# Optimization experiments

Measured on AMD Instinct MI355X. Metric: run time of the kernel, lower is better.

Reference implementation:

```python
import jax, jax.numpy as jnp
import numpy as np

THRESHOLD = 0.3
NEG_BIG = -2.0 ** 32  # matches tf -2**32 causal mask constant


def setup_inputs() -> dict:
    key = jax.random.key(0)
    kq, kt, kv = jax.random.split(key, 3)
    B, S, D = 16, 2048, 128
    Q = jax.random.normal(kq, (B, S, D), dtype=jnp.float32)
    T = jax.random.normal(kt, (B, S, D), dtype=jnp.float32)
    V = jax.random.normal(kv, (B, S, D), dtype=jnp.float32)
    return {"Q": Q, "T": T, "V": V}


def reference(Q, T, V):
    # scores: [B, S, S]
    A = jnp.einsum('bqd,bkd->bqk', Q, T)
    # Faithful to tf.where(A>thr, A, -2**32 * cast(A>thr)):
    # the false branch evaluates to 0 (mask is 0 there), NOT -2**32.
    A = jnp.where(A > THRESHOLD, A, jnp.zeros((), A.dtype))
    S = Q.shape[1]
    causal = jnp.triu(jnp.ones((S, S), dtype=bool), k=1)  # strictly upper = masked
    A = A + jnp.where(causal, jnp.asarray(NEG_BIG, A.dtype), jnp.zeros((), A.dtype))
    d_k = jnp.asarray(Q.shape[-1], A.dtype)
    A = A / jnp.sqrt(d_k)
    y = jax.nn.softmax(A, axis=-1)
    return jnp.einsum('bqk,bkd->bqd', y, V)
```

## Files before the change

### kernel.cpp

```cpp
#include <hip/hip_runtime.h>
#include <hip/hip_bf16.h>


#define S_LEN 2048
#define D_DIM 128
#define BQ 64
#define BK 64
#define THRESH 0.3f
#define SCALE 0.08838834764831845f

typedef __bf16 bf16x8 __attribute__((ext_vector_type(8)));
typedef float f32x4 __attribute__((ext_vector_type(4)));

#define GLD16(g, l)                                                         \
    __builtin_amdgcn_global_load_lds(                                       \
        (const __attribute__((address_space(1))) unsigned int*)(g),         \
        (__attribute__((address_space(3))) unsigned int*)(l), 16, 0, 0)

__global__ void prep_kernel(const float* __restrict__ V, const float* __restrict__ T,
                            __bf16* __restrict__ Vt, __bf16* __restrict__ Tb) {
    __shared__ float tile[64][65];
    int bid = blockIdx.x;
    int tid = threadIdx.x;
    int b  = bid >> 6;
    int t2 = bid & 63;

    {
        int flat = tid * 16;
        int r = flat >> 7, cc = flat & 127;
        const float* p = T + ((size_t)b * S_LEN + t2 * 32 + r) * D_DIM + cc;
        __bf16* q = Tb + ((size_t)b * S_LEN + t2 * 32 + r) * D_DIM + cc;
        bf16x8 w0, w1;
        f32x4 a0 = *(const f32x4*)p,       a1 = *(const f32x4*)(p + 4);
        f32x4 a2 = *(const f32x4*)(p + 8), a3 = *(const f32x4*)(p + 12);
        #pragma unroll
        for (int j = 0; j < 4; ++j) {
            w0[j] = (__bf16)a0[j]; w0[4 + j] = (__bf16)a1[j];
            w1[j] = (__bf16)a2[j]; w1[4 + j] = (__bf16)a3[j];
        }
        *(bf16x8*)q = w0;
        *(bf16x8*)(q + 8) = w1;
    }

    int s0 = (t2 >> 1) * 64;
    int d0 = (t2 & 1) * 64;
    #pragma unroll
    for (int it = 0; it < 2; ++it) {
        int row = it * 32 + (tid >> 3);
        int c   = (tid & 7) * 8;
        const float* p = V + ((size_t)b * S_LEN + s0 + row) * D_DIM + d0 + c;
        *(f32x4*)(&tile[row][c])     = *(const f32x4*)p;
        *(f32x4*)(&tile[row][c + 4]) = *(const f32x4*)(p + 4);
    }
    __syncthreads();
    #pragma unroll
    for (int it = 0; it < 2; ++it) {
        int dr = it * 32 + (tid >> 3);
        int c  = (tid & 7) * 8;
        bf16x8 w;
        #pragma unroll
        for (int j = 0; j < 8; ++j) w[j] = (__bf16)tile[c + j][dr];
        *(bf16x8*)(Vt + ((size_t)b * D_DIM + d0 + dr) * S_LEN + s0 + c) = w;
    }
}

__global__ __launch_bounds__(256, 2)
void fa_kernel(const float* __restrict__ Q, const __bf16* __restrict__ Tb,
               const __bf16* __restrict__ Vt, float* __restrict__ O,
               float* __restrict__ pO, float* __restrict__ pL) {
    __shared__ __align__(16) unsigned char smem[73728];

    const int bid = blockIdx.x;
    const int b   = bid & 15;
    const int pi  = (bid >> 4) & 15;
    const int c   = bid >> 8;
    const int qtH = 31 - pi;
    const int L   = pi + 1;

    const int tid  = threadIdx.x;
    const int lane = tid & 63;
    const int wv   = tid >> 6;
    const int col  = lane & 15;
    const int quad = lane >> 4;

    unsigned char* Pw = smem + 65536 + wv * 2048;

    const __bf16* TbB = Tb + (size_t)b * S_LEN * D_DIM;
    const __bf16* VtB = Vt + (size_t)b * D_DIM * S_LEN;

    int toff[4], voff[4];
    #pragma unroll
    for (int i = 0; i < 4; ++i) {
        int trw = wv * 16 + i * 4 + (lane >> 4);
        toff[i] = trw * 128 + (((lane & 15) ^ (trw & 7)) << 3);
        int drw = wv * 32 + i * 8 + (lane >> 3);
        voff[i] = drw * 2048 + (((lane & 7) ^ (drw & 7)) << 3);
    }

    auto issueTile = [&](int k0, int buf) {
        const __bf16* ts = TbB + (size_t)k0 * D_DIM;
        const __bf16* vs = VtB + k0;
        unsigned char* lt = smem + buf * 16384 + wv * 4096;
        unsigned char* lv = smem + 32768 + buf * 16384 + wv * 4096;
        #pragma unroll
        for (int i = 0; i < 4; ++i) GLD16(ts + toff[i], lt + i * 1024);
        #pragma unroll
        for (int i = 0; i < 4; ++i) GLD16(vs + voff[i], lv + i * 1024);
    };

    bf16x8 qf[4];
    auto loadQ = [&](int qt) {
        const float* qptr = Q + ((size_t)b * S_LEN + qt * BQ + wv * 16 + col) * D_DIM + quad * 8;
        #pragma unroll
        for (int kk = 0; kk < 4; ++kk) {
            f32x4 a = *(const f32x4*)(qptr + kk * 32);
            f32x4 d = *(const f32x4*)(qptr + kk * 32 + 4);
            #pragma unroll
            for (int j = 0; j < 4; ++j) { qf[kk][j] = (__bf16)a[j]; qf[kk][4 + j] = (__bf16)d[j]; }
        }
    };

    f32x4 oacc[8];
    float lsum[4];

    auto computeTile = [&](int buf, bool diag) {
        unsigned char* Tt = smem + buf * 16384;
        unsigned char* Vl = smem + 32768 + buf * 16384;
        f32x4 sacc[4];
        __builtin_amdgcn_s_setprio(1);
        #pragma unroll
        for (int t = 0; t < 4; ++t) {
            sacc[t] = {0.f, 0.f, 0.f, 0.f};
            #pragma unroll
            for (int kk = 0; kk < 4; ++kk) {
                int row = t * 16 + col;
                bf16x8 bf = *(const bf16x8*)(Tt + row * 256 + ((kk * 64 + quad * 16) ^ ((row & 7) << 4)));
                sacc[t] = __builtin_amdgcn_mfma_f32_16x16x32_bf16(qf[kk], bf, sacc[t], 0, 0, 0);
            }
        }
        __builtin_amdgcn_s_setprio(0);
        float p[4][4];
        #pragma unroll
        for (int t = 0; t < 4; ++t)
            #pragma unroll
            for (int r = 0; r < 4; ++r) {
                float s = sacc[t][r];
                float e = __expf(s * SCALE);
                float w = (s > THRESH) ? e : 1.0f;
                if (diag && (t * 16 + col > wv * 16 + quad * 4 + r)) w = 0.0f;
                p[t][r] = w;
            }
        #pragma unroll
        for (int r = 0; r < 4; ++r)
            lsum[r] += (p[0][r] + p[1][r]) + (p[2][r] + p[3][r]);

        #pragma unroll
        for (int t = 0; t < 4; ++t)
            #pragma unroll
            for (int r = 0; r < 4; ++r) {
                int row = quad * 4 + r;
                *(__bf16*)(Pw + row * 128 + (((t * 16 + col) * 2) ^ ((row & 7) << 4))) = (__bf16)p[t][r];
            }
        asm volatile("s_waitcnt lgkmcnt(0)" ::: "memory");

        __builtin_amdgcn_s_setprio(1);
        #pragma unroll
        for (int ks = 0; ks < 2; ++ks) {
            bf16x8 af = *(const bf16x8*)(Pw + col * 128 + ((ks * 64 + quad * 16) ^ ((col & 7) << 4)));
            #pragma unroll
            for (int dt = 0; dt < 8; ++dt) {
                int row = dt * 16 + col;
                bf16x8 bf = *(const bf16x8*)(Vl + row * 128 + ((ks * 64 + quad * 16) ^ ((row & 7) << 4)));
                oacc[dt] = __builtin_amdgcn_mfma_f32_16x16x32_bf16(af, bf, oacc[dt], 0, 0, 0);
            }
        }
        __builtin_amdgcn_s_setprio(0);
    };

    auto finishSeg = [&](int qt) {
        float lred[4];
        #pragma unroll
        for (int r = 0; r < 4; ++r) {
            float l = lsum[r];
            l += __shfl_xor(l, 1); l += __shfl_xor(l, 2);
            l += __shfl_xor(l, 4); l += __shfl_xor(l, 8);
            lred[r] = l;
        }
        if (qt < 16) {
            float* optr = O + ((size_t)b * S_LEN + qt * BQ + wv * 16) * D_DIM;
            #pragma unroll
            for (int dt = 0; dt < 8; ++dt)
                #pragma unroll
                for (int r = 0; r < 4; ++r)
                    optr[(quad * 4 + r) * D_DIM + dt * 16 + col] = oacc[dt][r] * (1.0f / lred[r]);
        } else {
            size_t slot = (size_t)((b * 16 + pi) * 2 + c);
            float* po = pO + slot * (64 * 128);
            float* pl = pL + slot * 64;
            #pragma unroll
            for (int dt = 0; dt < 8; ++dt)
                #pragma unroll
                for (int r = 0; r < 4; ++r)
                    po[(wv * 16 + quad * 4 + r) * 128 + dt * 16 + col] = oacc[dt][r];
            if (col == 0) {
                #pragma unroll
                for (int r = 0; r < 4; ++r) pl[wv * 16 + quad * 4 + r] = lred[r];
            }
        }
    };

    const int nseg = (c == 0) ? 2 : 1;
    for (int is = 0; is < nseg; ++is) {
        int qt, k0t, nt;
        if (c == 0) {
            if (is == 0) { qt = pi;  k0t = 0;      nt = L;      }
            else         { qt = qtH; k0t = 0;      nt = 17 - L; }
        } else           { qt = qtH; k0t = 17 - L; nt = 16;     }

        loadQ(qt);
        #pragma unroll
        for (int dt = 0; dt < 8; ++dt) oacc[dt] = {0.f, 0.f, 0.f, 0.f};
        #pragma unroll
        for (int r = 0; r < 4; ++r) lsum[r] = 0.f;

        issueTile(k0t * BK, 0);
        for (int s = 0; s < nt; ++s) {
            if (s + 1 < nt) {
                issueTile((k0t + s + 1) * BK, (s + 1) & 1);
                asm volatile("s_waitcnt vmcnt(8)" ::: "memory");
            } else {
                asm volatile("s_waitcnt vmcnt(0)" ::: "memory");
            }
            __builtin_amdgcn_s_barrier();
            computeTile(s & 1, k0t + s == qt);
            __builtin_amdgcn_s_barrier();
        }
        finishSeg(qt);
    }
}

__global__ void nrm_kernel(const float* __restrict__ pO, const float* __restrict__ pL,
                           float* __restrict__ O) {
    int gid  = blockIdx.x * 256 + threadIdx.x;
    int flat = gid * 16;
    int pr   = flat >> 13;
    int rl   = (flat >> 7) & 63;
    int cc   = flat & 127;
    int b = pr >> 4, pi = pr & 15;
    const float* p0 = pO + ((size_t)pr * 2)     * 8192 + rl * 128 + cc;
    const float* p1 = pO + ((size_t)pr * 2 + 1) * 8192 + rl * 128 + cc;
    float inv = 1.0f / (pL[(pr * 2) * 64 + rl] + pL[(pr * 2 + 1) * 64 + rl]);
    float* op = O + ((size_t)b * S_LEN + (31 - pi) * 64 + rl) * D_DIM + cc;
    #pragma unroll
    for (int j = 0; j < 4; ++j) {
        f32x4 a = *(const f32x4*)(p0 + j * 4);
        f32x4 d = *(const f32x4*)(p1 + j * 4);
        f32x4 o;
        #pragma unroll
        for (int r = 0; r < 4; ++r) o[r] = (a[r] + d[r]) * inv;
        *(f32x4*)(op + j * 4) = o;
    }
}

extern "C" void kernel_launch(void* const* d_in, const int* in_sizes, int n_in,
                              void* d_out, int out_size, void* d_ws, size_t ws_size,
                              hipStream_t stream) {
    const float* Q = (const float*)d_in[0];
    const float* T = (const float*)d_in[1];
    const float* V = (const float*)d_in[2];
    float* O = (float*)d_out;

    unsigned char* ws = (unsigned char*)d_ws;
    __bf16* Vt = (__bf16*)ws;
    __bf16* Tb = (__bf16*)(ws + 8388608);
    float*  pO = (float*)(ws + 16777216);
    float*  pL = (float*)(ws + 16777216 + 16777216);

    prep_kernel<<<1024, 256, 0, stream>>>(V, T, Vt, Tb);
    fa_kernel<<<512, 256, 0, stream>>>(Q, Tb, Vt, O, pO, pL);
    nrm_kernel<<<512, 256, 0, stream>>>(pO, pL, O);
}
```

Measured before the change: 132.4 us.

## Switch to 32x32 MFMA with 128-row query tiles and in-kernel split-K reduction

Moves the attention kernel from 16x16x32 to 32x32x16 bf16 MFMA with 128-query-row tiles per block. The P tile now stays in registers as the A operand instead of round-tripping through LDS. The work split changes to four chunks per query-pair, and partial outputs are stored in bf16. The separate normalization kernel is gone: the last block spin-waits on atomic counters (zeroed in prep) and sums the partials itself. This removes a launch and fp32 partial traffic, but adds inter-block spin-waiting that could deadlock if blocks are not co-resident, plus bf16 rounding of the partials.

```diff
diff --git a/kernel.cpp b/kernel.cpp
--- a/kernel.cpp
+++ b/kernel.cpp
@@ -4,13 +4,14 @@
 
 #define S_LEN 2048
 #define D_DIM 128
-#define BQ 64
-#define BK 64
 #define THRESH 0.3f
 #define SCALE 0.08838834764831845f
 
 typedef __bf16 bf16x8 __attribute__((ext_vector_type(8)));
 typedef float f32x4 __attribute__((ext_vector_type(4)));
+typedef float f32x16 __attribute__((ext_vector_type(16)));
+typedef unsigned long long u64;
+typedef unsigned long long u64x2 __attribute__((ext_vector_type(2)));
 
 #define GLD16(g, l)                                                         \
     __builtin_amdgcn_global_load_lds(                                       \
@@ -18,10 +19,12 @@
         (__attribute__((address_space(3))) unsigned int*)(l), 16, 0, 0)
 
 __global__ void prep_kernel(const float* __restrict__ V, const float* __restrict__ T,
-                            __bf16* __restrict__ Vt, __bf16* __restrict__ Tb) {
+                            __bf16* __restrict__ Vt, __bf16* __restrict__ Tb,
+                            int* __restrict__ done) {
     __shared__ float tile[64][65];
     int bid = blockIdx.x;
     int tid = threadIdx.x;
+    if (bid == 0) done[tid] = 0;
     int b  = bid >> 6;
     int t2 = bid & 63;
 
@@ -67,26 +70,25 @@
 __global__ __launch_bounds__(256, 2)
 void fa_kernel(const float* __restrict__ Q, const __bf16* __restrict__ Tb,
                const __bf16* __restrict__ Vt, float* __restrict__ O,
-               float* __restrict__ pO, float* __restrict__ pL) {
-    __shared__ __align__(16) unsigned char smem[73728];
+               __bf16* __restrict__ pO, float* __restrict__ pL,
+               int* __restrict__ done) {
+    __shared__ __align__(16) unsigned char smem[65536];
 
     const int bid = blockIdx.x;
     const int b   = bid & 15;
-    const int pi  = (bid >> 4) & 15;
-    const int c   = bid >> 8;
-    const int qtH = 31 - pi;
-    const int L   = pi + 1;
+    const int pi  = (bid >> 4) & 7;
+    const int c   = bid >> 7;
+    const int L2  = 2 * pi + 2;
+    const int pr  = b * 8 + pi;
 
     const int tid  = threadIdx.x;
     const int lane = tid & 63;
     const int wv   = tid >> 6;
-    const int col  = lane & 15;
-    const int quad = lane >> 4;
-
-    unsigned char* Pw = smem + 65536 + wv * 2048;
-
-    const __bf16* TbB = Tb + (size_t)b * S_LEN * D_DIM;
-    const __bf16* VtB = Vt + (size_t)b * D_DIM * S_LEN;
+    const int l31  = lane & 31;
+    const int hi   = lane >> 5;
+
+    const __bf16* TbB = Tb + (size_t)b * (S_LEN * D_DIM);
+    const __bf16* VtB = Vt + (size_t)b * (D_DIM * S_LEN);
 
     int toff[4], voff[4];
     #pragma unroll
@@ -108,157 +110,196 @@
         for (int i = 0; i < 4; ++i) GLD16(vs + voff[i], lv + i * 1024);
     };
 
-    bf16x8 qf[4];
-    auto loadQ = [&](int qt) {
-        const float* qptr = Q + ((size_t)b * S_LEN + qt * BQ + wv * 16 + col) * D_DIM + quad * 8;
-        #pragma unroll
-        for (int kk = 0; kk < 4; ++kk) {
-            f32x4 a = *(const f32x4*)(qptr + kk * 32);
-            f32x4 d = *(const f32x4*)(qptr + kk * 32 + 4);
+    bf16x8 qf[8];
+    auto loadQ = [&](int jq) {
+        const float* qptr = Q + ((size_t)b * S_LEN + jq * 128 + wv * 32 + l31) * D_DIM + hi * 8;
+        #pragma unroll
+        for (int kk = 0; kk < 8; ++kk) {
+            f32x4 a = *(const f32x4*)(qptr + kk * 16);
+            f32x4 d = *(const f32x4*)(qptr + kk * 16 + 4);
             #pragma unroll
             for (int j = 0; j < 4; ++j) { qf[kk][j] = (__bf16)a[j]; qf[kk][4 + j] = (__bf16)d[j]; }
         }
     };
 
-    f32x4 oacc[8];
-    float lsum[4];
-
-    auto computeTile = [&](int buf, bool diag) {
+    f32x16 oacc[4];
+    float  lsum;
+
+    auto computeTile = [&](int buf, int jq, int kt) {
         unsigned char* Tt = smem + buf * 16384;
         unsigned char* Vl = smem + 32768 + buf * 16384;
-        f32x4 sacc[4];
+        f32x16 sacc0 = {}, sacc1 = {};
         __builtin_amdgcn_s_setprio(1);
         #pragma unroll
-        for (int t = 0; t < 4; ++t) {
-            sacc[t] = {0.f, 0.f, 0.f, 0.f};
-            #pragma unroll
-            for (int kk = 0; kk < 4; ++kk) {
-                int row = t * 16 + col;
-                bf16x8 bf = *(const bf16x8*)(Tt + row * 256 + ((kk * 64 + quad * 16) ^ ((row & 7) << 4)));
-                sacc[t] = __builtin_amdgcn_mfma_f32_16x16x32_bf16(qf[kk], bf, sacc[t], 0, 0, 0);
+        for (int kk = 0; kk < 8; ++kk) {
+            int r0 = l31;
+            bf16x8 tf0 = *(const bf16x8*)(Tt + r0 * 256 + ((kk * 32 + hi * 16) ^ ((r0 & 7) << 4)));
+            sacc0 = __builtin_amdgcn_mfma_f32_32x32x16_bf16(tf0, qf[kk], sacc0, 0, 0, 0);
+            int r1 = 32 + l31;
+            bf16x8 tf1 = *(const bf16x8*)(Tt + r1 * 256 + ((kk * 32 + hi * 16) ^ ((r1 & 7) << 4)));
+            sacc1 = __builtin_amdgcn_mfma_f32_32x32x16_bf16(tf1, qf[kk], sacc1, 0, 0, 0);
+        }
+        __builtin_amdgcn_s_setprio(0);
+
+        const int qin = wv * 32 + l31;
+        const int dK  = 128 * jq - 64 * kt;
+        float p[2][16];
+        #pragma unroll
+        for (int g = 0; g < 16; ++g) {
+            float s0 = sacc0[g], s1 = sacc1[g];
+            float e0 = __expf(s0 * SCALE), e1 = __expf(s1 * SCALE);
+            p[0][g] = (s0 > THRESH) ? e0 : 1.0f;
+            p[1][g] = (s1 > THRESH) ? e1 : 1.0f;
+        }
+        if (dK < 64) {
+            #pragma unroll
+            for (int t = 0; t < 2; ++t)
+                #pragma unroll
+                for (int g = 0; g < 16; ++g) {
+                    int key = t * 32 + (g & 3) + 8 * (g >> 2) + 4 * hi;
+                    if (key - qin > dK) p[t][g] = 0.0f;
+                }
+        }
+        float ls = 0.f;
+        #pragma unroll
+        for (int g = 0; g < 16; ++g) ls += (p[0][g] + p[1][g]);
+        lsum += ls;
+
+        bf16x8 pka[4];
+        #pragma unroll
+        for (int ks = 0; ks < 4; ++ks)
+            #pragma unroll
+            for (int j = 0; j < 8; ++j)
+                pka[ks][j] = (__bf16)p[ks >> 1][8 * (ks & 1) + j];
+
+        __builtin_amdgcn_s_setprio(1);
+        #pragma unroll
+        for (int ks = 0; ks < 4; ++ks) {
+            #pragma unroll
+            for (int dt = 0; dt < 4; ++dt) {
+                int d = dt * 32 + l31;
+                u64x2 vv;
+                vv[0] = *(const u64*)(Vl + d * 128 + ((((2 * ks)     ^ (d & 7)) << 4) + 8 * hi));
+                vv[1] = *(const u64*)(Vl + d * 128 + ((((2 * ks + 1) ^ (d & 7)) << 4) + 8 * hi));
+                bf16x8 vf = __builtin_bit_cast(bf16x8, vv);
+                oacc[dt] = __builtin_amdgcn_mfma_f32_32x32x16_bf16(pka[ks], vf, oacc[dt], 0, 0, 0);
             }
         }
         __builtin_amdgcn_s_setprio(0);
-        float p[4][4];
-        #pragma unroll
-        for (int t = 0; t < 4; ++t)
-            #pragma unroll
-            for (int r = 0; r < 4; ++r) {
-                float s = sacc[t][r];
-                float e = __expf(s * SCALE);
-                float w = (s > THRESH) ? e : 1.0f;
-                if (diag && (t * 16 + col > wv * 16 + quad * 4 + r)) w = 0.0f;
-                p[t][r] = w;
-            }
-        #pragma unroll
-        for (int r = 0; r < 4; ++r)
-            lsum[r] += (p[0][r] + p[1][r]) + (p[2][r] + p[3][r]);
-
-        #pragma unroll
-        for (int t = 0; t < 4; ++t)
-            #pragma unroll
-            for (int r = 0; r < 4; ++r) {
-                int row = quad * 4 + r;
-                *(__bf16*)(Pw + row * 128 + (((t * 16 + col) * 2) ^ ((row & 7) << 4))) = (__bf16)p[t][r];
-            }
-        asm volatile("s_waitcnt lgkmcnt(0)" ::: "memory");
-
-        __builtin_amdgcn_s_setprio(1);
-        #pragma unroll
-        for (int ks = 0; ks < 2; ++ks) {
-            bf16x8 af = *(const bf16x8*)(Pw + col * 128 + ((ks * 64 + quad * 16) ^ ((col & 7) << 4)));
-            #pragma unroll
-            for (int dt = 0; dt < 8; ++dt) {
-                int row = dt * 16 + col;
-                bf16x8 bf = *(const bf16x8*)(Vl + row * 128 + ((ks * 64 + quad * 16) ^ ((row & 7) << 4)));
-                oacc[dt] = __builtin_amdgcn_mfma_f32_16x16x32_bf16(af, bf, oacc[dt], 0, 0, 0);
-            }
-        }
-        __builtin_amdgcn_s_setprio(0);
-    };
-
-    auto finishSeg = [&](int qt) {
-        float lred[4];
-        #pragma unroll
-        for (int r = 0; r < 4; ++r) {
-            float l = lsum[r];
-            l += __shfl_xor(l, 1); l += __shfl_xor(l, 2);
-            l += __shfl_xor(l, 4); l += __shfl_xor(l, 8);
-            lred[r] = l;
-        }
-        if (qt < 16) {
-            float* optr = O + ((size_t)b * S_LEN + qt * BQ + wv * 16) * D_DIM;
-            #pragma unroll
-            for (int dt = 0; dt < 8; ++dt)
-                #pragma unroll
-                for (int r = 0; r < 4; ++r)
-                    optr[(quad * 4 + r) * D_DIM + dt * 16 + col] = oacc[dt][r] * (1.0f / lred[r]);
-        } else {
-            size_t slot = (size_t)((b * 16 + pi) * 2 + c);
-            float* po = pO + slot * (64 * 128);
-            float* pl = pL + slot * 64;
-            #pragma unroll
-            for (int dt = 0; dt < 8; ++dt)
-                #pragma unroll
-                for (int r = 0; r < 4; ++r)
-                    po[(wv * 16 + quad * 4 + r) * 128 + dt * 16 + col] = oacc[dt][r];
-            if (col == 0) {
-                #pragma unroll
-                for (int r = 0; r < 4; ++r) pl[wv * 16 + quad * 4 + r] = lred[r];
-            }
-        }
-    };
-
-    const int nseg = (c == 0) ? 2 : 1;
-    for (int is = 0; is < nseg; ++is) {
-        int qt, k0t, nt;
-        if (c == 0) {
-            if (is == 0) { qt = pi;  k0t = 0;      nt = L;      }
-            else         { qt = qtH; k0t = 0;      nt = 17 - L; }
-        } else           { qt = qtH; k0t = 17 - L; nt = 16;     }
-
-        loadQ(qt);
-        #pragma unroll
-        for (int dt = 0; dt < 8; ++dt) oacc[dt] = {0.f, 0.f, 0.f, 0.f};
-        #pragma unroll
-        for (int r = 0; r < 4; ++r) lsum[r] = 0.f;
-
-        issueTile(k0t * BK, 0);
+    };
+
+    auto runSeg = [&](int jq, int k0t, int nt) {
+        loadQ(jq);
+        f32x16 z = {};
+        #pragma unroll
+        for (int dt = 0; dt < 4; ++dt) oacc[dt] = z;
+        lsum = 0.f;
+        issueTile(k0t * 64, 0);
         for (int s = 0; s < nt; ++s) {
             if (s + 1 < nt) {
-                issueTile((k0t + s + 1) * BK, (s + 1) & 1);
+                issueTile((k0t + s + 1) * 64, (s + 1) & 1);
                 asm volatile("s_waitcnt vmcnt(8)" ::: "memory");
             } else {
                 asm volatile("s_waitcnt vmcnt(0)" ::: "memory");
             }
             __builtin_amdgcn_s_barrier();
-            computeTile(s & 1, k0t + s == qt);
+            computeTile(s & 1, jq, k0t + s);
             __builtin_amdgcn_s_barrier();
         }
-        finishSeg(qt);
-    }
-}
-
-__global__ void nrm_kernel(const float* __restrict__ pO, const float* __restrict__ pL,
-                           float* __restrict__ O) {
-    int gid  = blockIdx.x * 256 + threadIdx.x;
-    int flat = gid * 16;
-    int pr   = flat >> 13;
-    int rl   = (flat >> 7) & 63;
-    int cc   = flat & 127;
-    int b = pr >> 4, pi = pr & 15;
-    const float* p0 = pO + ((size_t)pr * 2)     * 8192 + rl * 128 + cc;
-    const float* p1 = pO + ((size_t)pr * 2 + 1) * 8192 + rl * 128 + cc;
-    float inv = 1.0f / (pL[(pr * 2) * 64 + rl] + pL[(pr * 2 + 1) * 64 + rl]);
-    float* op = O + ((size_t)b * S_LEN + (31 - pi) * 64 + rl) * D_DIM + cc;
-    #pragma unroll
-    for (int j = 0; j < 4; ++j) {
-        f32x4 a = *(const f32x4*)(p0 + j * 4);
-        f32x4 d = *(const f32x4*)(p1 + j * 4);
-        f32x4 o;
-        #pragma unroll
-        for (int r = 0; r < 4; ++r) o[r] = (a[r] + d[r]) * inv;
-        *(f32x4*)(op + j * 4) = o;
+    };
+
+    auto reduceL = [&]() -> float { return lsum + __shfl_xor(lsum, 32); };
+
+    auto storeOfinal = [&](int jq, float l_all) {
+        float linv = 1.0f / l_all;
+        float* optr = O + ((size_t)b * S_LEN + jq * 128 + wv * 32) * D_DIM;
+        #pragma unroll
+        for (int g = 0; g < 16; ++g) {
+            int ql = (g & 3) + 8 * (g >> 2) + 4 * hi;
+            float iv = __shfl(linv, ql);
+            #pragma unroll
+            for (int dt = 0; dt < 4; ++dt)
+                optr[ql * D_DIM + dt * 32 + l31] = oacc[dt][g] * iv;
+        }
+    };
+
+    auto storePartial = [&](int slot, float l_all, int* dcnt) {
+        __bf16* po = pO + (size_t)(pr * 3 + slot) * (128 * 128);
+        float*  pl = pL + (size_t)(pr * 3 + slot) * 128;
+        #pragma unroll
+        for (int g = 0; g < 16; ++g) {
+            int row = wv * 32 + (g & 3) + 8 * (g >> 2) + 4 * hi;
+            #pragma unroll
+            for (int dt = 0; dt < 4; ++dt)
+                po[row * 128 + dt * 32 + l31] = (__bf16)oacc[dt][g];
+        }
+        if (lane < 32) pl[wv * 32 + lane] = l_all;
+        __threadfence();
+        __syncthreads();
+        if (tid == 0)
+            __hip_atomic_fetch_add(dcnt, 1, __ATOMIC_RELEASE, __HIP_MEMORY_SCOPE_AGENT);
+    };
+
+    auto addPartial = [&](int slot, float* l_all) {
+        const __bf16* po = pO + (size_t)(pr * 3 + slot) * (128 * 128);
+        const float*  pl = pL + (size_t)(pr * 3 + slot) * 128;
+        #pragma unroll
+        for (int g = 0; g < 16; ++g) {
+            int row = wv * 32 + (g & 3) + 8 * (g >> 2) + 4 * hi;
+            #pragma unroll
+            for (int dt = 0; dt < 4; ++dt)
+                oacc[dt][g] += (float)po[row * 128 + dt * 32 + l31];
+        }
+        *l_all += pl[wv * 32 + l31];
+    };
+
+    auto spinFor = [&](int* dcnt, int need) {
+        if (tid == 0) {
+            while (__hip_atomic_load(dcnt, __ATOMIC_ACQUIRE, __HIP_MEMORY_SCOPE_AGENT) < need)
+                __builtin_amdgcn_s_sleep(8);
+        }
+        __syncthreads();
+        __threadfence();
+    };
+
+    if (c == 0) {
+        if (pi <= 3) {
+            runSeg(pi, 0, L2);
+            storeOfinal(pi, reduceL());
+            runSeg(15 - pi, 0, 9 - L2);
+            float lh = reduceL();
+            storePartial(0, lh, &done[128 + pr]);
+        } else {
+            runSeg(pi, 0, 9);
+            float la = reduceL();
+            storePartial(0, la, &done[pr]);
+        }
+    } else if (c == 1) {
+        if (pi <= 3) {
+            runSeg(15 - pi, 9 - L2, 8);
+            float lh = reduceL();
+            storePartial(1, lh, &done[128 + pr]);
+        } else {
+            runSeg(15 - pi, 0, 17 - L2);
+            float lh = reduceL();
+            storePartial(1, lh, &done[128 + pr]);
+            runSeg(pi, 9, L2 - 9);
+            float la = reduceL();
+            spinFor(&done[pr], 1);
+            addPartial(0, &la);
+            storeOfinal(pi, la);
+        }
+    } else if (c == 2) {
+        runSeg(15 - pi, 17 - L2, 9);
+        float lh = reduceL();
+        storePartial(2, lh, &done[128 + pr]);
+    } else {
+        runSeg(15 - pi, 26 - L2, 8);
+        float lh = reduceL();
+        int s0 = (pi <= 3) ? 0 : 1;
+        spinFor(&done[128 + pr], 3 - s0);
+        for (int s = s0; s < 3; ++s) addPartial(s, &lh);
+        storeOfinal(15 - pi, lh);
     }
 }
 
@@ -273,10 +314,10 @@
     unsigned char* ws = (unsigned char*)d_ws;
     __bf16* Vt = (__bf16*)ws;
     __bf16* Tb = (__bf16*)(ws + 8388608);
-    float*  pO = (float*)(ws + 16777216);
-    float*  pL = (float*)(ws + 16777216 + 16777216);
-
-    prep_kernel<<<1024, 256, 0, stream>>>(V, T, Vt, Tb);
-    fa_kernel<<<512, 256, 0, stream>>>(Q, Tb, Vt, O, pO, pL);
-    nrm_kernel<<<512, 256, 0, stream>>>(pO, pL, O);
+    __bf16* pO = (__bf16*)(ws + 16777216);
+    float*  pL = (float*)(ws + 16777216 + 12582912);
+    int*  done = (int*)(ws + 16777216 + 12582912 + 196608);
+
+    prep_kernel<<<1024, 256, 0, stream>>>(V, T, Vt, Tb, done);
+    fa_kernel<<<512, 256, 0, stream>>>(Q, Tb, Vt, O, pO, pL, done);
 }
```

Result: slower. 205.5 us (+55.2%).

## Use 128-row query tiles with 8 waves and in-kernel split-K reduction via atomics

Applied to the files above, without the earlier changes.

Each block now uses 512 threads and covers a 128-row query tile, with work split into four chunks per pair of low/high query tiles. Partial outputs are written in bf16, and a completion counter plus spin-wait lets the last block merge them in-kernel, which removes the separate normalization kernel. The larger Q tile halves how often T/V tiles are reloaded, and the bf16 partials cut workspace traffic. The costs are 80KB of LDS, spin-wait dependencies that rely on the producer blocks being co-resident, and reduced precision in the partial sums.

```diff
diff --git a/kernel.cpp b/kernel.cpp
--- a/kernel.cpp
+++ b/kernel.cpp
@@ -4,8 +4,6 @@
 
 #define S_LEN 2048
 #define D_DIM 128
-#define BQ 64
-#define BK 64
 #define THRESH 0.3f
 #define SCALE 0.08838834764831845f
 
@@ -18,10 +16,12 @@
         (__attribute__((address_space(3))) unsigned int*)(l), 16, 0, 0)
 
 __global__ void prep_kernel(const float* __restrict__ V, const float* __restrict__ T,
-                            __bf16* __restrict__ Vt, __bf16* __restrict__ Tb) {
+                            __bf16* __restrict__ Vt, __bf16* __restrict__ Tb,
+                            int* __restrict__ done) {
     __shared__ float tile[64][65];
     int bid = blockIdx.x;
     int tid = threadIdx.x;
+    if (bid == 0) done[tid] = 0;
     int b  = bid >> 6;
     int t2 = bid & 63;
 
@@ -64,18 +64,20 @@
     }
 }
 
-__global__ __launch_bounds__(256, 2)
+__global__ __launch_bounds__(512, 4)
 void fa_kernel(const float* __restrict__ Q, const __bf16* __restrict__ Tb,
                const __bf16* __restrict__ Vt, float* __restrict__ O,
-               float* __restrict__ pO, float* __restrict__ pL) {
-    __shared__ __align__(16) unsigned char smem[73728];
+               __bf16* __restrict__ pO, float* __restrict__ pL,
+               int* __restrict__ done) {
+    __shared__ __align__(16) unsigned char smem[81920];
 
     const int bid = blockIdx.x;
     const int b   = bid & 15;
-    const int pi  = (bid >> 4) & 15;
-    const int c   = bid >> 8;
-    const int qtH = 31 - pi;
-    const int L   = pi + 1;
+    const int pi  = (bid >> 4) & 7;
+    const int c   = bid >> 7;
+    const int L2  = 2 * pi + 2;
+    const int pr  = b * 8 + pi;
+    const int qtL = pi, qtH = 15 - pi;
 
     const int tid  = threadIdx.x;
     const int lane = tid & 63;
@@ -84,33 +86,32 @@
     const int quad = lane >> 4;
 
     unsigned char* Pw = smem + 65536 + wv * 2048;
-
-    const __bf16* TbB = Tb + (size_t)b * S_LEN * D_DIM;
-    const __bf16* VtB = Vt + (size_t)b * D_DIM * S_LEN;
-
-    int toff[4], voff[4];
+    const __bf16* TbB = Tb + (size_t)b * (S_LEN * D_DIM);
+    const __bf16* VtB = Vt + (size_t)b * (D_DIM * S_LEN);
+
+    int toff[2], voff[2];
     #pragma unroll
-    for (int i = 0; i < 4; ++i) {
-        int trw = wv * 16 + i * 4 + (lane >> 4);
+    for (int i = 0; i < 2; ++i) {
+        int trw = wv * 8 + i * 4 + (lane >> 4);
         toff[i] = trw * 128 + (((lane & 15) ^ (trw & 7)) << 3);
-        int drw = wv * 32 + i * 8 + (lane >> 3);
+        int drw = wv * 16 + i * 8 + (lane >> 3);
         voff[i] = drw * 2048 + (((lane & 7) ^ (drw & 7)) << 3);
     }
 
     auto issueTile = [&](int k0, int buf) {
         const __bf16* ts = TbB + (size_t)k0 * D_DIM;
         const __bf16* vs = VtB + k0;
-        unsigned char* lt = smem + buf * 16384 + wv * 4096;
-        unsigned char* lv = smem + 32768 + buf * 16384 + wv * 4096;
-        #pragma unroll
-        for (int i = 0; i < 4; ++i) GLD16(ts + toff[i], lt + i * 1024);
-        #pragma unroll
-        for (int i = 0; i < 4; ++i) GLD16(vs + voff[i], lv + i * 1024);
+        unsigned char* lt = smem + buf * 16384 + wv * 2048;
+        unsigned char* lv = smem + 32768 + buf * 16384 + wv * 2048;
+        GLD16(ts + toff[0], lt);
+        GLD16(ts + toff[1], lt + 1024);
+        GLD16(vs + voff[0], lv);
+        GLD16(vs + voff[1], lv + 1024);
     };
 
     bf16x8 qf[4];
-    auto loadQ = [&](int qt) {
-        const float* qptr = Q + ((size_t)b * S_LEN + qt * BQ + wv * 16 + col) * D_DIM + quad * 8;
+    auto loadQ = [&](int jq) {
+        const float* qptr = Q + ((size_t)b * S_LEN + jq * 128 + wv * 16 + col) * D_DIM + quad * 8;
         #pragma unroll
         for (int kk = 0; kk < 4; ++kk) {
             f32x4 a = *(const f32x4*)(qptr + kk * 32);
@@ -123,7 +124,7 @@
     f32x4 oacc[8];
     float lsum[4];
 
-    auto computeTile = [&](int buf, bool diag) {
+    auto computeTile = [&](int buf, int dK) {
         unsigned char* Tt = smem + buf * 16384;
         unsigned char* Vl = smem + 32768 + buf * 16384;
         f32x4 sacc[4];
@@ -146,10 +147,15 @@
             for (int r = 0; r < 4; ++r) {
                 float s = sacc[t][r];
                 float e = __expf(s * SCALE);
-                float w = (s > THRESH) ? e : 1.0f;
-                if (diag && (t * 16 + col > wv * 16 + quad * 4 + r)) w = 0.0f;
-                p[t][r] = w;
-            }
+                p[t][r] = (s > THRESH) ? e : 1.0f;
+            }
+        if (dK < 64) {
+            #pragma unroll
+            for (int t = 0; t < 4; ++t)
+                #pragma unroll
+                for (int r = 0; r < 4; ++r)
+                    if (t * 16 + col - (wv * 16 + quad * 4 + r) > dK) p[t][r] = 0.0f;
+        }
         #pragma unroll
         for (int r = 0; r < 4; ++r)
             lsum[r] += (p[0][r] + p[1][r]) + (p[2][r] + p[3][r]);
@@ -177,8 +183,28 @@
         __builtin_amdgcn_s_setprio(0);
     };
 
-    auto finishSeg = [&](int qt) {
-        float lred[4];
+    auto runSeg = [&](int jq, int k0t, int nt) {
+        loadQ(jq);
+        #pragma unroll
+        for (int dt = 0; dt < 8; ++dt) oacc[dt] = {0.f, 0.f, 0.f, 0.f};
+        #pragma unroll
+        for (int r = 0; r < 4; ++r) lsum[r] = 0.f;
+        issueTile(k0t * 64, 0);
+        for (int s = 0; s < nt; ++s) {
+            if (s + 1 < nt) {
+                issueTile((k0t + s + 1) * 64, (s + 1) & 1);
+                asm volatile("s_waitcnt vmcnt(4)" ::: "memory");
+            } else {
+                asm volatile("s_waitcnt vmcnt(0)" ::: "memory");
+            }
+            __builtin_amdgcn_s_barrier();
+            computeTile(s & 1, 128 * jq - 64 * (k0t + s));
+            __builtin_amdgcn_s_barrier();
+        }
+    };
+
+    float lred[4];
+    auto reduceL = [&]() {
         #pragma unroll
         for (int r = 0; r < 4; ++r) {
             float l = lsum[r];
@@ -186,79 +212,97 @@
             l += __shfl_xor(l, 4); l += __shfl_xor(l, 8);
             lred[r] = l;
         }
-        if (qt < 16) {
-            float* optr = O + ((size_t)b * S_LEN + qt * BQ + wv * 16) * D_DIM;
+    };
+
+    auto storeO = [&](int jq) {
+        float* optr = O + ((size_t)b * S_LEN + jq * 128 + wv * 16) * D_DIM;
+        #pragma unroll
+        for (int r = 0; r < 4; ++r) {
+            float inv = 1.0f / lred[r];
             #pragma unroll
             for (int dt = 0; dt < 8; ++dt)
-                #pragma unroll
-                for (int r = 0; r < 4; ++r)
-                    optr[(quad * 4 + r) * D_DIM + dt * 16 + col] = oacc[dt][r] * (1.0f / lred[r]);
+                optr[(quad * 4 + r) * D_DIM + dt * 16 + col] = oacc[dt][r] * inv;
+        }
+    };
+
+    auto storePartial = [&](int slot, int* dcnt) {
+        __bf16* po = pO + (size_t)(pr * 4 + slot) * (128 * 128);
+        float*  pl = pL + (size_t)(pr * 4 + slot) * 128;
+        #pragma unroll
+        for (int dt = 0; dt < 8; ++dt)
+            #pragma unroll
+            for (int r = 0; r < 4; ++r)
+                po[(wv * 16 + quad * 4 + r) * 128 + dt * 16 + col] = (__bf16)oacc[dt][r];
+        if (col == 0) {
+            #pragma unroll
+            for (int r = 0; r < 4; ++r) pl[wv * 16 + quad * 4 + r] = lred[r];
+        }
+        __threadfence();
+        __syncthreads();
+        if (tid == 0)
+            __hip_atomic_fetch_add(dcnt, 1, __ATOMIC_RELEASE, __HIP_MEMORY_SCOPE_AGENT);
+    };
+
+    auto addPartial = [&](int slot) {
+        const __bf16* po = pO + (size_t)(pr * 4 + slot) * (128 * 128);
+        const float*  pl = pL + (size_t)(pr * 4 + slot) * 128;
+        #pragma unroll
+        for (int dt = 0; dt < 8; ++dt)
+            #pragma unroll
+            for (int r = 0; r < 4; ++r)
+                oacc[dt][r] += (float)po[(wv * 16 + quad * 4 + r) * 128 + dt * 16 + col];
+        #pragma unroll
+        for (int r = 0; r < 4; ++r) lred[r] += pl[wv * 16 + quad * 4 + r];
+    };
+
+    auto spinFor = [&](int* dcnt, int need) {
+        if (tid == 0) {
+            while (__hip_atomic_load(dcnt, __ATOMIC_ACQUIRE, __HIP_MEMORY_SCOPE_AGENT) < need)
+                __builtin_amdgcn_s_sleep(8);
+        }
+        __syncthreads();
+        __threadfence();
+    };
+
+    if (c == 0) {
+        if (pi <= 3) {
+            runSeg(qtL, 0, L2);
+            reduceL();
+            storeO(qtL);
+            runSeg(qtH, 0, 9 - L2);
+            reduceL();
+            storePartial(0, &done[128 + pr]);
         } else {
-            size_t slot = (size_t)((b * 16 + pi) * 2 + c);
-            float* po = pO + slot * (64 * 128);
-            float* pl = pL + slot * 64;
-            #pragma unroll
-            for (int dt = 0; dt < 8; ++dt)
-                #pragma unroll
-                for (int r = 0; r < 4; ++r)
-                    po[(wv * 16 + quad * 4 + r) * 128 + dt * 16 + col] = oacc[dt][r];
-            if (col == 0) {
-                #pragma unroll
-                for (int r = 0; r < 4; ++r) pl[wv * 16 + quad * 4 + r] = lred[r];
-            }
-        }
-    };
-
-    const int nseg = (c == 0) ? 2 : 1;
-    for (int is = 0; is < nseg; ++is) {
-        int qt, k0t, nt;
-        if (c == 0) {
-            if (is == 0) { qt = pi;  k0t = 0;      nt = L;      }
-            else         { qt = qtH; k0t = 0;      nt = 17 - L; }
-        } else           { qt = qtH; k0t = 17 - L; nt = 16;     }
-
-        loadQ(qt);
-        #pragma unroll
-        for (int dt = 0; dt < 8; ++dt) oacc[dt] = {0.f, 0.f, 0.f, 0.f};
-        #pragma unroll
-        for (int r = 0; r < 4; ++r) lsum[r] = 0.f;
-
-        issueTile(k0t * BK, 0);
-        for (int s = 0; s < nt; ++s) {
-            if (s + 1 < nt) {
-                issueTile((k0t + s + 1) * BK, (s + 1) & 1);
-                asm volatile("s_waitcnt vmcnt(8)" ::: "memory");
-            } else {
-                asm volatile("s_waitcnt vmcnt(0)" ::: "memory");
-            }
-            __builtin_amdgcn_s_barrier();
-            computeTile(s & 1, k0t + s == qt);
-            __builtin_amdgcn_s_barrier();
-        }
-        finishSeg(qt);
-    }
-}
-
-__global__ void nrm_kernel(const float* __restrict__ pO, const float* __restrict__ pL,
-                           float* __restrict__ O) {
-    int gid  = blockIdx.x * 256 + threadIdx.x;
-    int flat = gid * 16;
-    int pr   = flat >> 13;
-    int rl   = (flat >> 7) & 63;
-    int cc   = flat & 127;
-    int b = pr >> 4, pi = pr & 15;
-    const float* p0 = pO + ((size_t)pr * 2)     * 8192 + rl * 128 + cc;
-    const float* p1 = pO + ((size_t)pr * 2 + 1) * 8192 + rl * 128 + cc;
-    float inv = 1.0f / (pL[(pr * 2) * 64 + rl] + pL[(pr * 2 + 1) * 64 + rl]);
-    float* op = O + ((size_t)b * S_LEN + (31 - pi) * 64 + rl) * D_DIM + cc;
-    #pragma unroll
-    for (int j = 0; j < 4; ++j) {
-        f32x4 a = *(const f32x4*)(p0 + j * 4);
-        f32x4 d = *(const f32x4*)(p1 + j * 4);
-        f32x4 o;
-        #pragma unroll
-        for (int r = 0; r < 4; ++r) o[r] = (a[r] + d[r]) * inv;
-        *(f32x4*)(op + j * 4) = o;
+            runSeg(qtL, 0, 9);
+            reduceL();
+            storePartial(3, &done[pr]);
+        }
+    } else if (c == 1) {
+        if (pi <= 3) {
+            runSeg(qtH, 9 - L2, 8);
+            reduceL();
+            storePartial(1, &done[128 + pr]);
+        } else {
+            runSeg(qtH, 0, 17 - L2);
+            reduceL();
+            storePartial(1, &done[128 + pr]);
+            runSeg(qtL, 9, L2 - 9);
+            reduceL();
+            spinFor(&done[pr], 1);
+            addPartial(3);
+            storeO(qtL);
+        }
+    } else if (c == 2) {
+        runSeg(qtH, 17 - L2, 9);
+        reduceL();
+        storePartial(2, &done[128 + pr]);
+    } else {
+        runSeg(qtH, 26 - L2, 8);
+        reduceL();
+        int s0 = (pi <= 3) ? 0 : 1;
+        spinFor(&done[128 + pr], 3 - s0);
+        for (int s = s0; s < 3; ++s) addPartial(s);
+        storeO(qtH);
     }
 }
 
@@ -273,10 +317,10 @@
     unsigned char* ws = (unsigned char*)d_ws;
     __bf16* Vt = (__bf16*)ws;
     __bf16* Tb = (__bf16*)(ws + 8388608);
-    float*  pO = (float*)(ws + 16777216);
+    __bf16* pO = (__bf16*)(ws + 16777216);
     float*  pL = (float*)(ws + 16777216 + 16777216);
-
-    prep_kernel<<<1024, 256, 0, stream>>>(V, T, Vt, Tb);
-    fa_kernel<<<512, 256, 0, stream>>>(Q, Tb, Vt, O, pO, pL);
-    nrm_kernel<<<512, 256, 0, stream>>>(pO, pL, O);
+    int*  done = (int*)(ws + 16777216 + 16777216 + 262144);
+
+    prep_kernel<<<1024, 256, 0, stream>>>(V, T, Vt, Tb, done);
+    fa_kernel<<<512, 512, 0, stream>>>(Q, Tb, Vt, O, pO, pL, done);
 }
```

Result: slower. 317.0 us (+139.4%).

## Repartition attention tile so each wave owns key columns and D-slice

Applied to the files above, without the earlier changes.

Work is re-split across the four waves. Each wave now computes transposed scores for its own 16 keys against all 64 queries, with Q held in registers for all four query sub-tiles. P is written to one shared LDS tile, and each wave then computes a 32-wide slice of the output D dimension for all queries. This cuts per-wave LDS reads of T and V fragments and reuses each loaded fragment across four MFMAs. In exchange it adds an extra block barrier per tile, a cross-wave row-sum reduction through LDS, and higher register pressure from 16 Q fragments.

```diff
diff --git a/kernel.cpp b/kernel.cpp
--- a/kernel.cpp
+++ b/kernel.cpp
@@ -4,12 +4,11 @@
 
 #define S_LEN 2048
 #define D_DIM 128
-#define BQ 64
-#define BK 64
 #define THRESH 0.3f
 #define SCALE 0.08838834764831845f
 
 typedef __bf16 bf16x8 __attribute__((ext_vector_type(8)));
+typedef __bf16 bf16x4 __attribute__((ext_vector_type(4)));
 typedef float f32x4 __attribute__((ext_vector_type(4)));
 
 #define GLD16(g, l)                                                         \
@@ -83,10 +82,11 @@
     const int col  = lane & 15;
     const int quad = lane >> 4;
 
-    unsigned char* Pw = smem + 65536 + wv * 2048;
-
-    const __bf16* TbB = Tb + (size_t)b * S_LEN * D_DIM;
-    const __bf16* VtB = Vt + (size_t)b * D_DIM * S_LEN;
+    unsigned char* Pb = smem + 65536;
+    float* Lxf = (float*)(smem + 65536);
+
+    const __bf16* TbB = Tb + (size_t)b * (S_LEN * D_DIM);
+    const __bf16* VtB = Vt + (size_t)b * (D_DIM * S_LEN);
 
     int toff[4], voff[4];
     #pragma unroll
@@ -108,37 +108,43 @@
         for (int i = 0; i < 4; ++i) GLD16(vs + voff[i], lv + i * 1024);
     };
 
-    bf16x8 qf[4];
-    auto loadQ = [&](int qt) {
-        const float* qptr = Q + ((size_t)b * S_LEN + qt * BQ + wv * 16 + col) * D_DIM + quad * 8;
-        #pragma unroll
-        for (int kk = 0; kk < 4; ++kk) {
-            f32x4 a = *(const f32x4*)(qptr + kk * 32);
-            f32x4 d = *(const f32x4*)(qptr + kk * 32 + 4);
-            #pragma unroll
-            for (int j = 0; j < 4; ++j) { qf[kk][j] = (__bf16)a[j]; qf[kk][4 + j] = (__bf16)d[j]; }
-        }
-    };
-
-    f32x4 oacc[8];
+    bf16x8 qf[4][4];
+    auto loadQ = [&](int jq) {
+        #pragma unroll
+        for (int t = 0; t < 4; ++t) {
+            const float* qptr = Q + ((size_t)b * S_LEN + jq * 64 + 16 * t + col) * D_DIM + quad * 8;
+            #pragma unroll
+            for (int kk = 0; kk < 4; ++kk) {
+                f32x4 a = *(const f32x4*)(qptr + kk * 32);
+                f32x4 d = *(const f32x4*)(qptr + kk * 32 + 4);
+                #pragma unroll
+                for (int j = 0; j < 4; ++j) { qf[t][kk][j] = (__bf16)a[j]; qf[t][kk][4 + j] = (__bf16)d[j]; }
+            }
+        }
+    };
+
+    f32x4 oacc[4][2];
     float lsum[4];
+    float lfull[4][4];
 
     auto computeTile = [&](int buf, bool diag) {
         unsigned char* Tt = smem + buf * 16384;
         unsigned char* Vl = smem + 32768 + buf * 16384;
+
         f32x4 sacc[4];
+        #pragma unroll
+        for (int t = 0; t < 4; ++t) sacc[t] = {0.f, 0.f, 0.f, 0.f};
         __builtin_amdgcn_s_setprio(1);
         #pragma unroll
-        for (int t = 0; t < 4; ++t) {
-            sacc[t] = {0.f, 0.f, 0.f, 0.f};
-            #pragma unroll
-            for (int kk = 0; kk < 4; ++kk) {
-                int row = t * 16 + col;
-                bf16x8 bf = *(const bf16x8*)(Tt + row * 256 + ((kk * 64 + quad * 16) ^ ((row & 7) << 4)));
-                sacc[t] = __builtin_amdgcn_mfma_f32_16x16x32_bf16(qf[kk], bf, sacc[t], 0, 0, 0);
-            }
+        for (int kk = 0; kk < 4; ++kk) {
+            int trow = wv * 16 + col;
+            bf16x8 tf = *(const bf16x8*)(Tt + trow * 256 + ((kk * 64 + quad * 16) ^ ((trow & 7) << 4)));
+            #pragma unroll
+            for (int t = 0; t < 4; ++t)
+                sacc[t] = __builtin_amdgcn_mfma_f32_16x16x32_bf16(tf, qf[t][kk], sacc[t], 0, 0, 0);
         }
         __builtin_amdgcn_s_setprio(0);
+
         float p[4][4];
         #pragma unroll
         for (int t = 0; t < 4; ++t)
@@ -146,96 +152,134 @@
             for (int r = 0; r < 4; ++r) {
                 float s = sacc[t][r];
                 float e = __expf(s * SCALE);
-                float w = (s > THRESH) ? e : 1.0f;
-                if (diag && (t * 16 + col > wv * 16 + quad * 4 + r)) w = 0.0f;
-                p[t][r] = w;
-            }
-        #pragma unroll
-        for (int r = 0; r < 4; ++r)
-            lsum[r] += (p[0][r] + p[1][r]) + (p[2][r] + p[3][r]);
-
-        #pragma unroll
-        for (int t = 0; t < 4; ++t)
-            #pragma unroll
-            for (int r = 0; r < 4; ++r) {
-                int row = quad * 4 + r;
-                *(__bf16*)(Pw + row * 128 + (((t * 16 + col) * 2) ^ ((row & 7) << 4))) = (__bf16)p[t][r];
-            }
+                p[t][r] = (s > THRESH) ? e : 1.0f;
+            }
+        if (diag) {
+            #pragma unroll
+            for (int t = 0; t < 4; ++t)
+                #pragma unroll
+                for (int r = 0; r < 4; ++r)
+                    if (wv * 16 + quad * 4 + r > 16 * t + col) p[t][r] = 0.0f;
+        }
+        #pragma unroll
+        for (int t = 0; t < 4; ++t)
+            lsum[t] += (p[t][0] + p[t][1]) + (p[t][2] + p[t][3]);
+
+        #pragma unroll
+        for (int t = 0; t < 4; ++t) {
+            int row = 16 * t + col;
+            bf16x4 w = {(__bf16)p[t][0], (__bf16)p[t][1], (__bf16)p[t][2], (__bf16)p[t][3]};
+            *(bf16x4*)(Pb + row * 128 + ((32 * wv + 8 * quad) ^ ((row & 7) << 4))) = w;
+        }
         asm volatile("s_waitcnt lgkmcnt(0)" ::: "memory");
+        __builtin_amdgcn_s_barrier();
 
         __builtin_amdgcn_s_setprio(1);
         #pragma unroll
-        for (int ks = 0; ks < 2; ++ks) {
-            bf16x8 af = *(const bf16x8*)(Pw + col * 128 + ((ks * 64 + quad * 16) ^ ((col & 7) << 4)));
-            #pragma unroll
-            for (int dt = 0; dt < 8; ++dt) {
-                int row = dt * 16 + col;
-                bf16x8 bf = *(const bf16x8*)(Vl + row * 128 + ((ks * 64 + quad * 16) ^ ((row & 7) << 4)));
-                oacc[dt] = __builtin_amdgcn_mfma_f32_16x16x32_bf16(af, bf, oacc[dt], 0, 0, 0);
+        for (int kb = 0; kb < 2; ++kb) {
+            bf16x8 pf[4];
+            #pragma unroll
+            for (int t = 0; t < 4; ++t) {
+                int prow = 16 * t + col;
+                pf[t] = *(const bf16x8*)(Pb + prow * 128 + ((kb * 64 + quad * 16) ^ ((prow & 7) << 4)));
+            }
+            #pragma unroll
+            for (int dn = 0; dn < 2; ++dn) {
+                int vrow = 32 * wv + 16 * dn + col;
+                bf16x8 vf = *(const bf16x8*)(Vl + vrow * 128 + ((kb * 64 + quad * 16) ^ ((vrow & 7) << 4)));
+                #pragma unroll
+                for (int t = 0; t < 4; ++t)
+                    oacc[t][dn] = __builtin_amdgcn_mfma_f32_16x16x32_bf16(pf[t], vf, oacc[t][dn], 0, 0, 0);
             }
         }
         __builtin_amdgcn_s_setprio(0);
     };
 
-    auto finishSeg = [&](int qt) {
-        float lred[4];
-        #pragma unroll
-        for (int r = 0; r < 4; ++r) {
-            float l = lsum[r];
-            l += __shfl_xor(l, 1); l += __shfl_xor(l, 2);
-            l += __shfl_xor(l, 4); l += __shfl_xor(l, 8);
-            lred[r] = l;
-        }
-        if (qt < 16) {
-            float* optr = O + ((size_t)b * S_LEN + qt * BQ + wv * 16) * D_DIM;
-            #pragma unroll
-            for (int dt = 0; dt < 8; ++dt)
-                #pragma unroll
-                for (int r = 0; r < 4; ++r)
-                    optr[(quad * 4 + r) * D_DIM + dt * 16 + col] = oacc[dt][r] * (1.0f / lred[r]);
-        } else {
-            size_t slot = (size_t)((b * 16 + pi) * 2 + c);
-            float* po = pO + slot * (64 * 128);
-            float* pl = pL + slot * 64;
-            #pragma unroll
-            for (int dt = 0; dt < 8; ++dt)
-                #pragma unroll
-                for (int r = 0; r < 4; ++r)
-                    po[(wv * 16 + quad * 4 + r) * 128 + dt * 16 + col] = oacc[dt][r];
-            if (col == 0) {
-                #pragma unroll
-                for (int r = 0; r < 4; ++r) pl[wv * 16 + quad * 4 + r] = lred[r];
-            }
-        }
-    };
-
-    const int nseg = (c == 0) ? 2 : 1;
-    for (int is = 0; is < nseg; ++is) {
-        int qt, k0t, nt;
-        if (c == 0) {
-            if (is == 0) { qt = pi;  k0t = 0;      nt = L;      }
-            else         { qt = qtH; k0t = 0;      nt = 17 - L; }
-        } else           { qt = qtH; k0t = 17 - L; nt = 16;     }
-
-        loadQ(qt);
-        #pragma unroll
-        for (int dt = 0; dt < 8; ++dt) oacc[dt] = {0.f, 0.f, 0.f, 0.f};
-        #pragma unroll
-        for (int r = 0; r < 4; ++r) lsum[r] = 0.f;
-
-        issueTile(k0t * BK, 0);
+    auto runSeg = [&](int jq, int k0t, int nt) {
+        loadQ(jq);
+        #pragma unroll
+        for (int t = 0; t < 4; ++t) {
+            oacc[t][0] = {0.f, 0.f, 0.f, 0.f};
+            oacc[t][1] = {0.f, 0.f, 0.f, 0.f};
+            lsum[t] = 0.f;
+        }
+        issueTile(k0t * 64, 0);
         for (int s = 0; s < nt; ++s) {
             if (s + 1 < nt) {
-                issueTile((k0t + s + 1) * BK, (s + 1) & 1);
+                issueTile((k0t + s + 1) * 64, (s + 1) & 1);
                 asm volatile("s_waitcnt vmcnt(8)" ::: "memory");
             } else {
                 asm volatile("s_waitcnt vmcnt(0)" ::: "memory");
             }
             __builtin_amdgcn_s_barrier();
-            computeTile(s & 1, k0t + s == qt);
+            computeTile(s & 1, k0t + s == jq);
             __builtin_amdgcn_s_barrier();
         }
-        finishSeg(qt);
+    };
+
+    auto finishSeg = [&]() {
+        #pragma unroll
+        for (int t = 0; t < 4; ++t) {
+            float lw = lsum[t];
+            lw += __shfl_xor(lw, 16);
+            lw += __shfl_xor(lw, 32);
+            if (quad == 0) Lxf[wv * 64 + 16 * t + col] = lw;
+        }
+        __syncthreads();
+        #pragma unroll
+        for (int t = 0; t < 4; ++t)
+            #pragma unroll
+            for (int r = 0; r < 4; ++r) {
+                int q = 16 * t + quad * 4 + r;
+                lfull[t][r] = (Lxf[q] + Lxf[64 + q]) + (Lxf[128 + q] + Lxf[192 + q]);
+            }
+        __syncthreads();
+    };
+
+    auto storeO = [&](int jq) {
+        float* optr = O + ((size_t)b * S_LEN + jq * 64) * D_DIM;
+        #pragma unroll
+        for (int t = 0; t < 4; ++t)
+            #pragma unroll
+            for (int r = 0; r < 4; ++r) {
+                float inv = 1.0f / lfull[t][r];
+                #pragma unroll
+                for (int dn = 0; dn < 2; ++dn)
+                    optr[(16 * t + quad * 4 + r) * D_DIM + 32 * wv + 16 * dn + col] = oacc[t][dn][r] * inv;
+            }
+    };
+
+    auto storePartial = [&]() {
+        size_t slot = (size_t)((b * 16 + pi) * 2 + c);
+        float* po = pO + slot * (64 * 128);
+        float* pl = pL + slot * 64;
+        #pragma unroll
+        for (int t = 0; t < 4; ++t)
+            #pragma unroll
+            for (int r = 0; r < 4; ++r)
+                #pragma unroll
+                for (int dn = 0; dn < 2; ++dn)
+                    po[(16 * t + quad * 4 + r) * 128 + 32 * wv + 16 * dn + col] = oacc[t][dn][r];
+        if (wv == 0 && col == 0) {
+            #pragma unroll
+            for (int t = 0; t < 4; ++t)
+                #pragma unroll
+                for (int r = 0; r < 4; ++r)
+                    pl[16 * t + quad * 4 + r] = lfull[t][r];
+        }
+    };
+
+    if (c == 0) {
+        runSeg(pi, 0, L);
+        finishSeg();
+        storeO(pi);
+        runSeg(qtH, 0, 17 - L);
+        finishSeg();
+        storePartial();
+    } else {
+        runSeg(qtH, 17 - L, 16);
+        finishSeg();
+        storePartial();
     }
 }
 
```

Measured after the change: 131.4 us. About the same (-0.8%).
